# Performance work log

Measured on AMD Instinct MI355X. Metric: run time of the kernel, lower is better.

Reference implementation:

```python
import jax, jax.numpy as jnp
import numpy as np

V, D, H, L, MAXS = 32000, 768, 12, 6, 2048
HD = D // H  # 64
FF = 4 * D
B, S = 8, 1024
EPS = 1e-5


def _make_pe():
    pos = np.arange(MAXS, dtype=np.float32)[:, None]
    div = np.exp(np.arange(0, D, 2, dtype=np.float32) * (-np.log(10000.0) / D))
    pe = np.zeros((MAXS, D), dtype=np.float32)
    pe[:, 0::2] = np.sin(pos * div)
    pe[:, 1::2] = np.cos(pos * div)
    return jnp.asarray(pe)


def setup_inputs() -> dict:
    key = jax.random.key(0)
    ks = jax.random.split(key, 16)
    sc = 0.02
    return {
        "tokens": jax.random.randint(ks[0], (B, S), 0, V),
        "k_mask": jnp.ones((B, S), dtype=jnp.int32),
        "emb": jax.random.normal(ks[1], (V, D), jnp.float32) * sc,
        "pe": _make_pe(),
        "ln1_s": jnp.ones((L, D), jnp.float32),
        "ln1_b": jnp.zeros((L, D), jnp.float32),
        "wq": jax.random.normal(ks[2], (L, H, D, HD), jnp.float32) * sc,
        "wk": jax.random.normal(ks[3], (L, H, D, HD), jnp.float32) * sc,
        "wv": jax.random.normal(ks[4], (L, H, D, HD), jnp.float32) * sc,
        "wo": jax.random.normal(ks[5], (L, D, D), jnp.float32) * sc,
        "ln2_s": jnp.ones((L, D), jnp.float32),
        "ln2_b": jnp.zeros((L, D), jnp.float32),
        "w1": jax.random.normal(ks[6], (L, D, FF), jnp.float32) * sc,
        "b1": jnp.zeros((L, FF), jnp.float32),
        "w2": jax.random.normal(ks[7], (L, FF, D), jnp.float32) * sc,
        "b2": jnp.zeros((L, D), jnp.float32),
    }


def _ln(x, s, b):
    m = jnp.mean(x, axis=-1, keepdims=True)
    v = jnp.var(x, axis=-1, keepdims=True)
    return (x - m) * jax.lax.rsqrt(v + EPS) * s + b


def _forward(tokens, k_mask, emb, pe, ln1_s, ln1_b, wq, wk, wv, wo,
             ln2_s, ln2_b, w1, b1, w2, b2):
    x = emb[tokens] + pe[None, :tokens.shape[1], :]  # [B,S,D]
    mask = (k_mask != 0)[:, None, None, :]  # [B,1,1,S]
    for l in range(L):
        xn = _ln(x, ln1_s[l], ln1_b[l])
        q = jnp.einsum('bsd,hde->bhse', xn, wq[l])
        k = jnp.einsum('bsd,hde->bhse', xn, wk[l])
        v = jnp.einsum('bsd,hde->bhse', xn, wv[l])
        scores = jnp.einsum('bhse,bhte->bhst', q, k) / (HD ** 0.5)
        scores = jnp.where(mask, scores, -jnp.inf)
        attn = jax.nn.softmax(scores, axis=-1)
        o = jnp.einsum('bhst,bhte->bhse', attn, v)  # [B,H,S,HD]
        o = o.transpose(0, 2, 1, 3).reshape(x.shape)  # concat heads -> [B,S,D]
        x = x + o @ wo[l]
        xn = _ln(x, ln2_s[l], ln2_b[l])
        h = jax.nn.gelu(xn @ w1[l] + b1[l], approximate=False)
        x = x + h @ w2[l] + b2[l]
    return x


def reference(tokens, k_mask, emb, pe, ln1_s, ln1_b, wq, wk, wv, wo,
              ln2_s, ln2_b, w1, b1, w2, b2):
    return _forward(tokens, k_mask, emb, pe, ln1_s, ln1_b, wq, wk, wv, wo,
                    ln2_s, ln2_b, w1, b1, w2, b2)
```

## Files before the change

kernel.cpp:

```cpp
#include <hip/hip_runtime.h>
#include <math.h>

typedef unsigned short u16;
typedef unsigned int u32;
typedef __attribute__((ext_vector_type(8))) __bf16 bf16x8;
typedef __attribute__((ext_vector_type(4))) float f32x4;
typedef __attribute__((ext_vector_type(8))) unsigned short ushort8v;
typedef __attribute__((ext_vector_type(4))) float float4v;
typedef __attribute__((ext_vector_type(4))) unsigned short u16x4;

typedef const __attribute__((address_space(1))) void gvoid_t;
typedef __attribute__((address_space(3))) void lvoid_t;

#define MFMA(a, b, c) __builtin_amdgcn_mfma_f32_16x16x32_bf16((a), (b), (c), 0, 0, 0)

__device__ __forceinline__ u16 f2bf(float f) {
  __bf16 h = (__bf16)f;
  return __builtin_bit_cast(u16, h);
}

__device__ __forceinline__ void stage64(const u16* g, int ldg, u16* lds, int rows, int tid) {
  int w = tid >> 6, l = tid & 63;
  int lr = l >> 3;
  int cb = (l & 7) << 4;
  for (int it = 0; it < rows; it += 32) {
    int rbase = it + w * 8;
    int r = rbase + lr;
    int scb = cb ^ ((r & 7) << 4);
    const char* gp = (const char*)(g + (size_t)r * ldg) + scb;
    char* lp = (char*)lds + (size_t)rbase * 128;
    __builtin_amdgcn_global_load_lds((gvoid_t*)gp, (lvoid_t*)lp, 16, 0, 0);
  }
}

__device__ __forceinline__ bf16x8 ldsfrag(const u16* base, int row, int e0) {
  int boff = row * 128 + (((e0) << 1) ^ ((row & 7) << 4));
  return *(const bf16x8*)((const char*)base + boff);
}

__global__ void embed_kernel(const int* __restrict__ tok, const float* __restrict__ emb,
                             const float* __restrict__ pe, float* __restrict__ xf) {
  int row = blockIdx.x;
  int tid = threadIdx.x;
  int t = tok[row];
  int spos = row & 1023;
  float4v e = ((const float4v*)(emb + (size_t)t * 768))[tid];
  float4v p = ((const float4v*)(pe + (size_t)spos * 768))[tid];
  float4v r;
  r.x = e.x + p.x; r.y = e.y + p.y; r.z = e.z + p.z; r.w = e.w + p.w;
  ((float4v*)(xf + (size_t)row * 768))[tid] = r;
}

__global__ void ln_kernel(const float* __restrict__ x, const float* __restrict__ sc,
                          const float* __restrict__ bi, u16* __restrict__ out) {
  int row = blockIdx.x;
  int tid = threadIdx.x;
  float4v v = ((const float4v*)(x + (size_t)row * 768))[tid];
  float s = v.x + v.y + v.z + v.w;
  float s2 = v.x * v.x + v.y * v.y + v.z * v.z + v.w * v.w;
  #pragma unroll
  for (int off = 32; off >= 1; off >>= 1) {
    s += __shfl_down(s, off);
    s2 += __shfl_down(s2, off);
  }
  __shared__ float red[8];
  if ((tid & 63) == 0) { red[tid >> 6] = s; red[4 + (tid >> 6)] = s2; }
  __syncthreads();
  float S = red[0] + red[1] + red[2];
  float S2 = red[4] + red[5] + red[6];
  float m = S * (1.0f / 768.0f);
  float var = S2 * (1.0f / 768.0f) - m * m;
  float rs = rsqrtf(var + 1e-5f);
  float4v sv = ((const float4v*)sc)[tid];
  float4v bv = ((const float4v*)bi)[tid];
  u16x4 ov;
  ov.x = f2bf((v.x - m) * rs * sv.x + bv.x);
  ov.y = f2bf((v.y - m) * rs * sv.y + bv.y);
  ov.z = f2bf((v.z - m) * rs * sv.z + bv.z);
  ov.w = f2bf((v.w - m) * rs * sv.w + bv.w);
  *(u16x4*)(out + (size_t)row * 768 + tid * 4) = ov;
}

__global__ void convT_kernel(const float* __restrict__ src, u16* __restrict__ dst,
                             int N, int K, long long sz, long long dz) {
  src += (size_t)blockIdx.z * sz;
  dst += (size_t)blockIdx.z * dz;
  __shared__ float t[32][33];
  int n0 = blockIdx.x * 32, k0 = blockIdx.y * 32;
  int tid = threadIdx.x;
  int tx = tid & 31, ty = tid >> 5;
  for (int r = ty; r < 32; r += 8) t[r][tx] = src[(size_t)(k0 + r) * N + n0 + tx];
  __syncthreads();
  for (int r = ty; r < 32; r += 8) dst[(size_t)(n0 + r) * K + k0 + tx] = f2bf(t[tx][r]);
}

__global__ void convqkvT_kernel(const float* __restrict__ wq, const float* __restrict__ wk,
                                const float* __restrict__ wv, u16* __restrict__ dst,
                                long long wz, long long dz) {
  __shared__ float t[32][33];
  int n0 = blockIdx.x * 32, k0 = blockIdx.y * 32;
  int which = n0 / 768;
  int r0 = n0 % 768;
  int h = r0 >> 6, e0 = r0 & 63;
  const float* src = which == 0 ? wq : (which == 1 ? wk : wv);
  src += (size_t)blockIdx.z * wz;
  dst += (size_t)blockIdx.z * dz;
  int tid = threadIdx.x;
  int tx = tid & 31, ty = tid >> 5;
  for (int r = ty; r < 32; r += 8) t[r][tx] = src[(size_t)(h * 768 + k0 + r) * 64 + e0 + tx];
  __syncthreads();
  for (int r = ty; r < 32; r += 8) dst[(size_t)(n0 + r) * 768 + k0 + tx] = f2bf(t[tx][r]);
}

__global__ void transpose_v_kernel(const u16* __restrict__ v, u16* __restrict__ vt) {
  __shared__ u16 t[64][72];
  int bh = blockIdx.x, sc = blockIdx.y;
  int tid = threadIdx.x;
  const u16* src = v + ((size_t)bh * 1024 + sc * 64) * 64;
  int sl = tid >> 2, e0 = (tid & 3) * 16;
  ushort8v a = *(const ushort8v*)(src + (size_t)sl * 64 + e0);
  ushort8v b = *(const ushort8v*)(src + (size_t)sl * 64 + e0 + 8);
  #pragma unroll
  for (int j = 0; j < 8; ++j) t[sl][e0 + j] = a[j];
  #pragma unroll
  for (int j = 0; j < 8; ++j) t[sl][e0 + 8 + j] = b[j];
  __syncthreads();
  int e = tid >> 2, s0 = (tid & 3) * 16;
  ushort8v o0, o1;
  #pragma unroll
  for (int j = 0; j < 8; ++j) o0[j] = t[s0 + j][e];
  #pragma unroll
  for (int j = 0; j < 8; ++j) o1[j] = t[s0 + 8 + j][e];
  u16* dst = vt + ((size_t)bh * 64 + e) * 1024 + sc * 64 + s0;
  *(ushort8v*)dst = o0;
  *(ushort8v*)(dst + 8) = o1;
}

template <int MODE>
__global__ __launch_bounds__(256) void gemm128(
    const u16* __restrict__ A, int lda, const u16* __restrict__ Wt, int K,
    float* __restrict__ xf, u16* __restrict__ outb, const float* __restrict__ bias,
    u16* __restrict__ qb, u16* __restrict__ kb, u16* __restrict__ vb) {
  __shared__ alignas(16) u16 As[128 * 64];
  __shared__ alignas(16) u16 Bs[128 * 64];
  int tid = threadIdx.x, lane = tid & 63, w = tid >> 6;
  int wm = w >> 1, wn = w & 1;
  int m0 = blockIdx.x * 128, n0 = blockIdx.y * 128;
  f32x4 acc[4][4] = {};
  const u16* Ag = A + (size_t)m0 * lda;
  const u16* Bg = Wt + (size_t)n0 * K;
  int arow = wm * 64 + (lane & 15);
  int brow = wn * 64 + (lane & 15);
  int e0 = (lane >> 4) * 8;
  for (int kt = 0; kt < K; kt += 64) {
    __syncthreads();
    stage64(Ag + kt, lda, As, 128, tid);
    stage64(Bg + kt, K, Bs, 128, tid);
    __syncthreads();
    #pragma unroll
    for (int kk = 0; kk < 2; ++kk) {
      bf16x8 af[4], bfr[4];
      #pragma unroll
      for (int mt = 0; mt < 4; ++mt) af[mt] = ldsfrag(As, arow + mt * 16, kk * 32 + e0);
      #pragma unroll
      for (int nt = 0; nt < 4; ++nt) bfr[nt] = ldsfrag(Bs, brow + nt * 16, kk * 32 + e0);
      #pragma unroll
      for (int mt = 0; mt < 4; ++mt)
        #pragma unroll
        for (int nt = 0; nt < 4; ++nt)
          acc[mt][nt] = MFMA(af[mt], bfr[nt], acc[mt][nt]);
    }
  }
  int rbase = m0 + wm * 64 + ((lane >> 4) << 2);
  int cbase = n0 + wn * 64 + (lane & 15);
  if constexpr (MODE == 0) {
    int which = n0 / 768;
    u16* dstb = which == 0 ? qb : (which == 1 ? kb : vb);
    int cloc = cbase - which * 768;
    #pragma unroll
    for (int mt = 0; mt < 4; ++mt) {
      #pragma unroll
      for (int nt = 0; nt < 4; ++nt) {
        int rr = cloc + nt * 16;
        int h = rr >> 6, e = rr & 63;
        #pragma unroll
        for (int reg = 0; reg < 4; ++reg) {
          int row = rbase + mt * 16 + reg;
          int b = row >> 10, s = row & 1023;
          dstb[((size_t)(b * 12 + h) * 1024 + s) * 64 + e] = f2bf(acc[mt][nt][reg]);
        }
      }
    }
  } else {
    #pragma unroll
    for (int mt = 0; mt < 4; ++mt) {
      #pragma unroll
      for (int nt = 0; nt < 4; ++nt) {
        int col = cbase + nt * 16;
        #pragma unroll
        for (int reg = 0; reg < 4; ++reg) {
          int row = rbase + mt * 16 + reg;
          float val = acc[mt][nt][reg];
          if constexpr (MODE == 1) {
            xf[(size_t)row * 768 + col] += val;
          } else if constexpr (MODE == 2) {
            float t = val + bias[col];
            float u = t * fmaf(t * t, 0.044715f, 1.0f);
            float ex = __builtin_amdgcn_exp2f(u * -2.3022156f);
            float g = t * __builtin_amdgcn_rcpf(1.0f + ex);
            outb[(size_t)row * 3072 + col] = f2bf(g);
          } else {
            xf[(size_t)row * 768 + col] += val + bias[col];
          }
        }
      }
    }
  }
}

__global__ __launch_bounds__(256) void flash64(
    const u16* __restrict__ q, const u16* __restrict__ k, const u16* __restrict__ vt,
    const int* __restrict__ kmask, u16* __restrict__ o) {
  __shared__ alignas(16) u16 Qs[64 * 64];
  __shared__ alignas(16) u16 Ks[64 * 64];
  __shared__ alignas(16) u16 Vs[64 * 64];
  __shared__ alignas(16) u16 Ps[64 * 64];
  int tid = threadIdx.x, lane = tid & 63, w = tid >> 6;
  int lc = lane & 15;
  int bh = blockIdx.x, q0 = blockIdx.y * 64;
  int b = bh / 12, h = bh % 12;

  stage64(q + ((size_t)bh * 1024 + q0) * 64, 64, Qs, 64, tid);
  __syncthreads();
  int qrow = w * 16 + lc;
  int e0 = (lane >> 4) * 8;
  bf16x8 aq0 = ldsfrag(Qs, qrow, e0);
  bf16x8 aq1 = ldsfrag(Qs, qrow, 32 + e0);

  bf16x8 ones;
  #pragma unroll
  for (int j = 0; j < 8; ++j) ones[j] = (__bf16)1.0f;

  f32x4 oacc[4] = {};
  f32x4 lacc = {};
  const float SCL = 0.125f * 1.44269504f;
  const float SH = -3.0f * 1.44269504f;
  int prow_base = w * 16 + ((lane >> 4) << 2);

  for (int kt = 0; kt < 16; ++kt) {
    __syncthreads();
    stage64(k + ((size_t)bh * 1024 + kt * 64) * 64, 64, Ks, 64, tid);
    stage64(vt + (size_t)bh * 64 * 1024 + kt * 64, 1024, Vs, 64, tid);
    __syncthreads();

    f32x4 sacc[4] = {};
    #pragma unroll
    for (int nt = 0; nt < 4; ++nt) {
      bf16x8 bk = ldsfrag(Ks, nt * 16 + lc, e0);
      sacc[nt] = MFMA(aq0, bk, sacc[nt]);
    }
    #pragma unroll
    for (int nt = 0; nt < 4; ++nt) {
      bf16x8 bk = ldsfrag(Ks, nt * 16 + lc, 32 + e0);
      sacc[nt] = MFMA(aq1, bk, sacc[nt]);
    }

    #pragma unroll
    for (int nt = 0; nt < 4; ++nt) {
      int c = nt * 16 + lc;
      float mk = kmask[b * 1024 + kt * 64 + c] ? SH : -1e30f;
      #pragma unroll
      for (int r = 0; r < 4; ++r) {
        float p = __builtin_amdgcn_exp2f(fmaf(sacc[nt][r], SCL, mk));
        int prow = prow_base + r;
        int boff = prow * 128 + ((c << 1) ^ ((prow & 7) << 4));
        *(u16*)((char*)Ps + boff) = f2bf(p);
      }
    }

    bf16x8 ap0 = ldsfrag(Ps, qrow, e0);
    bf16x8 ap1 = ldsfrag(Ps, qrow, 32 + e0);
    lacc = MFMA(ap0, ones, lacc);
    lacc = MFMA(ap1, ones, lacc);
    #pragma unroll
    for (int et = 0; et < 4; ++et) {
      bf16x8 bv = ldsfrag(Vs, et * 16 + lc, e0);
      oacc[et] = MFMA(ap0, bv, oacc[et]);
    }
    #pragma unroll
    for (int et = 0; et < 4; ++et) {
      bf16x8 bv = ldsfrag(Vs, et * 16 + lc, 32 + e0);
      oacc[et] = MFMA(ap1, bv, oacc[et]);
    }
  }

  float rl[4];
  #pragma unroll
  for (int r = 0; r < 4; ++r) rl[r] = __builtin_amdgcn_rcpf(lacc[r]);
  int orow_base = q0 + prow_base;
  #pragma unroll
  for (int et = 0; et < 4; ++et) {
    int e = et * 16 + lc;
    #pragma unroll
    for (int r = 0; r < 4; ++r) {
      int row = orow_base + r;
      o[((size_t)(b * 1024 + row)) * 768 + h * 64 + e] = f2bf(oacc[et][r] * rl[r]);
    }
  }
}

__global__ void copy_kernel(const float* __restrict__ src, float* __restrict__ dst) {
  size_t i = (size_t)blockIdx.x * blockDim.x + threadIdx.x;
  ((float4v*)dst)[i] = ((const float4v*)src)[i];
}

extern "C" void kernel_launch(void* const* d_in, const int* in_sizes, int n_in,
                              void* d_out, int out_size, void* d_ws, size_t ws_size,
                              hipStream_t stream) {
  const int* tokens = (const int*)d_in[0];
  const int* kmask = (const int*)d_in[1];
  const float* emb = (const float*)d_in[2];
  const float* pe = (const float*)d_in[3];
  const float* ln1_s = (const float*)d_in[4];
  const float* ln1_b = (const float*)d_in[5];
  const float* wq = (const float*)d_in[6];
  const float* wk = (const float*)d_in[7];
  const float* wv = (const float*)d_in[8];
  const float* wo = (const float*)d_in[9];
  const float* ln2_s = (const float*)d_in[10];
  const float* ln2_b = (const float*)d_in[11];
  const float* w1 = (const float*)d_in[12];
  const float* b1 = (const float*)d_in[13];
  const float* w2 = (const float*)d_in[14];
  const float* b2 = (const float*)d_in[15];

  char* ws = (char*)d_ws;
  float* xf = (float*)ws;
  u16* xn   = (u16*)(ws + 25165824);
  u16* qb   = (u16*)(ws + 37748736);
  u16* kb   = (u16*)(ws + 50331648);
  u16* vb   = (u16*)(ws + 62914560);
  u16* vtb  = (u16*)(ws + 75497472);
  u16* ob   = (u16*)(ws + 88080384);
  u16* ffh  = (u16*)(ws + 100663296);

  const size_t SZ_QKV = (size_t)2304 * 768;
  const size_t SZ_O   = (size_t)768 * 768;
  const size_t SZ_F1  = (size_t)3072 * 768;
  const size_t SZ_F2  = (size_t)768 * 3072;
  const size_t NEED = 150994944 + 2 * 6 * (SZ_QKV + SZ_O + SZ_F1 + SZ_F2);
  bool pre = ws_size >= NEED;
  int nz = pre ? 6 : 1;
  u16* wqkvt = (u16*)(ws + 150994944);
  u16* wot   = wqkvt + (size_t)nz * SZ_QKV;
  u16* w1t   = wot + (size_t)nz * SZ_O;
  u16* w2t   = w1t + (size_t)nz * SZ_F1;

  embed_kernel<<<8192, 192, 0, stream>>>(tokens, emb, pe, xf);

  if (pre) {
    convqkvT_kernel<<<dim3(72, 24, 6), 256, 0, stream>>>(wq, wk, wv, wqkvt, 589824LL, (long long)SZ_QKV);
    convT_kernel<<<dim3(24, 24, 6), 256, 0, stream>>>(wo, wot, 768, 768, 589824LL, (long long)SZ_O);
    convT_kernel<<<dim3(96, 24, 6), 256, 0, stream>>>(w1, w1t, 3072, 768, 2359296LL, (long long)SZ_F1);
    convT_kernel<<<dim3(24, 96, 6), 256, 0, stream>>>(w2, w2t, 768, 3072, 2359296LL, (long long)SZ_F2);
  }

  for (int l = 0; l < 6; ++l) {
    size_t woff_qkv = (size_t)l * 12 * 768 * 64;
    size_t woff_o = (size_t)l * 768 * 768;
    size_t woff_ff = (size_t)l * 768 * 3072;
    const u16* wt_qkv_l = wqkvt + (pre ? (size_t)l * SZ_QKV : 0);
    const u16* wt_o_l   = wot   + (pre ? (size_t)l * SZ_O   : 0);
    const u16* wt_1_l   = w1t   + (pre ? (size_t)l * SZ_F1  : 0);
    const u16* wt_2_l   = w2t   + (pre ? (size_t)l * SZ_F2  : 0);

    if (!pre) {
      convqkvT_kernel<<<dim3(72, 24, 1), 256, 0, stream>>>(wq + woff_qkv, wk + woff_qkv, wv + woff_qkv, (u16*)wt_qkv_l, 0LL, 0LL);
      convT_kernel<<<dim3(24, 24, 1), 256, 0, stream>>>(wo + woff_o, (u16*)wt_o_l, 768, 768, 0LL, 0LL);
      convT_kernel<<<dim3(96, 24, 1), 256, 0, stream>>>(w1 + woff_ff, (u16*)wt_1_l, 3072, 768, 0LL, 0LL);
      convT_kernel<<<dim3(24, 96, 1), 256, 0, stream>>>(w2 + woff_ff, (u16*)wt_2_l, 768, 3072, 0LL, 0LL);
    }

    ln_kernel<<<8192, 192, 0, stream>>>(xf, ln1_s + l * 768, ln1_b + l * 768, xn);
    gemm128<0><<<dim3(64, 18), 256, 0, stream>>>(xn, 768, wt_qkv_l, 768, nullptr, nullptr, nullptr, qb, kb, vb);
    transpose_v_kernel<<<dim3(96, 16), 256, 0, stream>>>(vb, vtb);
    flash64<<<dim3(96, 16), 256, 0, stream>>>(qb, kb, vtb, kmask, ob);
    gemm128<1><<<dim3(64, 6), 256, 0, stream>>>(ob, 768, wt_o_l, 768, xf, nullptr, nullptr, nullptr, nullptr, nullptr);
    ln_kernel<<<8192, 192, 0, stream>>>(xf, ln2_s + l * 768, ln2_b + l * 768, xn);
    gemm128<2><<<dim3(64, 24), 256, 0, stream>>>(xn, 768, wt_1_l, 768, nullptr, ffh, b1 + l * 3072, nullptr, nullptr, nullptr);
    gemm128<3><<<dim3(64, 6), 256, 0, stream>>>(ffh, 3072, wt_2_l, 3072, xf, nullptr, b2 + l * 768, nullptr, nullptr, nullptr);
  }

  copy_kernel<<<6144, 256, 0, stream>>>(xf, (float*)d_out);
}
```

Baseline: 1.686 ms.

## Replace 128x128 GEMM with 256x256 multi-stage pipelined GEMM and split-K atomics

Replaces the 128x128 tile GEMM with a 256x256 tile, 512-thread kernel. It uses a 4-slot LDS ring with 3-stage-ahead global_load_lds prefetch, explicit vmcnt waits, and raised priority around the MFMA section. The residual-add GEMMs (attention output and FFN down projection) use split-K across three z-slices and accumulate into the fp32 residual with atomicAdd. The aim is more data reuse per tile, global loads overlapped with compute, and better occupancy for the small-N GEMMs. In exchange it adds atomic traffic, makes summation order nondeterministic, and drops the LDS swizzle, which may cause bank conflicts.

```diff
diff --git a/kernel.cpp b/kernel.cpp
--- a/kernel.cpp
+++ b/kernel.cpp
@@ -36,6 +36,17 @@
 __device__ __forceinline__ bf16x8 ldsfrag(const u16* base, int row, int e0) {
   int boff = row * 128 + (((e0) << 1) ^ ((row & 7) << 4));
   return *(const bf16x8*)((const char*)base + boff);
+}
+
+__device__ __forceinline__ void stage_slice512(const u16* g, int ldg, char* dst, int tid) {
+  int rr = tid >> 2, s = tid & 3;
+  char* lp = dst + (tid >> 6) * 1024;
+  #pragma unroll
+  for (int i = 0; i < 2; ++i) {
+    int row = i * 128 + rr;
+    const char* gp = (const char*)g + (size_t)row * (ldg * 2) + s * 16;
+    __builtin_amdgcn_global_load_lds((gvoid_t*)gp, (lvoid_t*)(lp + i * 8192), 16, 0, 0);
+  }
 }
 
 __global__ void embed_kernel(const int* __restrict__ tok, const float* __restrict__ emb,
@@ -137,51 +148,76 @@
 }
 
 template <int MODE>
-__global__ __launch_bounds__(256) void gemm128(
-    const u16* __restrict__ A, int lda, const u16* __restrict__ Wt, int K,
+__global__ __launch_bounds__(512, 1) void gemm256(
+    const u16* __restrict__ A, int lda, const u16* __restrict__ Wt, int ldb, int kChunk,
     float* __restrict__ xf, u16* __restrict__ outb, const float* __restrict__ bias,
     u16* __restrict__ qb, u16* __restrict__ kb, u16* __restrict__ vb) {
-  __shared__ alignas(16) u16 As[128 * 64];
-  __shared__ alignas(16) u16 Bs[128 * 64];
+  extern __shared__ char lds[];
   int tid = threadIdx.x, lane = tid & 63, w = tid >> 6;
-  int wm = w >> 1, wn = w & 1;
-  int m0 = blockIdx.x * 128, n0 = blockIdx.y * 128;
-  f32x4 acc[4][4] = {};
-  const u16* Ag = A + (size_t)m0 * lda;
-  const u16* Bg = Wt + (size_t)n0 * K;
-  int arow = wm * 64 + (lane & 15);
-  int brow = wn * 64 + (lane & 15);
-  int e0 = (lane >> 4) * 8;
-  for (int kt = 0; kt < K; kt += 64) {
-    __syncthreads();
-    stage64(Ag + kt, lda, As, 128, tid);
-    stage64(Bg + kt, K, Bs, 128, tid);
-    __syncthreads();
-    #pragma unroll
-    for (int kk = 0; kk < 2; ++kk) {
-      bf16x8 af[4], bfr[4];
+  int wm = w >> 2, wn = w & 3;
+  int m0 = blockIdx.x * 256, n0 = blockIdx.y * 256;
+  int kb0 = blockIdx.z * kChunk;
+  int NK = kChunk >> 5;
+  const u16* Ag = A + (size_t)m0 * lda + kb0;
+  const u16* Bg = Wt + (size_t)n0 * ldb + kb0;
+  f32x4 acc[8][4] = {};
+  int lcb = (lane >> 4) << 4;
+  int lc = lane & 15;
+
+  #pragma unroll
+  for (int p = 0; p < 3; ++p) {
+    stage_slice512(Ag + p * 32, lda, lds + (p & 3) * 32768, tid);
+    stage_slice512(Bg + p * 32, ldb, lds + (p & 3) * 32768 + 16384, tid);
+  }
+
+  for (int ks = 0; ks < NK; ++ks) {
+    int newer = NK - 1 - ks;
+    if (newer >= 2)      asm volatile("s_waitcnt vmcnt(8)" ::: "memory");
+    else if (newer == 1) asm volatile("s_waitcnt vmcnt(4)" ::: "memory");
+    else                 asm volatile("s_waitcnt vmcnt(0)" ::: "memory");
+    __builtin_amdgcn_sched_barrier(0);
+    __builtin_amdgcn_s_barrier();
+    __builtin_amdgcn_sched_barrier(0);
+
+    char* sa = lds + (ks & 3) * 32768;
+    char* sb = sa + 16384;
+    bf16x8 af[8], bfr[4];
+    #pragma unroll
+    for (int mt = 0; mt < 8; ++mt) {
+      int r = wm * 128 + mt * 16 + lc;
+      af[mt] = *(const bf16x8*)(sa + r * 64 + lcb);
+    }
+    #pragma unroll
+    for (int nt = 0; nt < 4; ++nt) {
+      int r = wn * 64 + nt * 16 + lc;
+      bfr[nt] = *(const bf16x8*)(sb + r * 64 + lcb);
+    }
+    if (ks + 3 < NK) {
+      stage_slice512(Ag + (ks + 3) * 32, lda, lds + ((ks + 3) & 3) * 32768, tid);
+      stage_slice512(Bg + (ks + 3) * 32, ldb, lds + ((ks + 3) & 3) * 32768 + 16384, tid);
+    }
+    asm volatile("s_waitcnt lgkmcnt(0)" ::: "memory");
+    __builtin_amdgcn_sched_barrier(0);
+    __builtin_amdgcn_s_setprio(1);
+    #pragma unroll
+    for (int mt = 0; mt < 8; ++mt)
       #pragma unroll
-      for (int mt = 0; mt < 4; ++mt) af[mt] = ldsfrag(As, arow + mt * 16, kk * 32 + e0);
-      #pragma unroll
-      for (int nt = 0; nt < 4; ++nt) bfr[nt] = ldsfrag(Bs, brow + nt * 16, kk * 32 + e0);
-      #pragma unroll
-      for (int mt = 0; mt < 4; ++mt)
-        #pragma unroll
-        for (int nt = 0; nt < 4; ++nt)
-          acc[mt][nt] = MFMA(af[mt], bfr[nt], acc[mt][nt]);
-    }
-  }
-  int rbase = m0 + wm * 64 + ((lane >> 4) << 2);
-  int cbase = n0 + wn * 64 + (lane & 15);
+      for (int nt = 0; nt < 4; ++nt)
+        acc[mt][nt] = MFMA(af[mt], bfr[nt], acc[mt][nt]);
+    __builtin_amdgcn_s_setprio(0);
+  }
+
+  int rbase = m0 + wm * 128 + ((lane >> 4) << 2);
+  int cbase = n0 + wn * 64 + lc;
   if constexpr (MODE == 0) {
     int which = n0 / 768;
     u16* dstb = which == 0 ? qb : (which == 1 ? kb : vb);
-    int cloc = cbase - which * 768;
-    #pragma unroll
-    for (int mt = 0; mt < 4; ++mt) {
+    int clocal = n0 - which * 768 + wn * 64 + lc;
+    #pragma unroll
+    for (int mt = 0; mt < 8; ++mt) {
       #pragma unroll
       for (int nt = 0; nt < 4; ++nt) {
-        int rr = cloc + nt * 16;
+        int rr = clocal + nt * 16;
         int h = rr >> 6, e = rr & 63;
         #pragma unroll
         for (int reg = 0; reg < 4; ++reg) {
@@ -191,27 +227,36 @@
         }
       }
     }
-  } else {
-    #pragma unroll
-    for (int mt = 0; mt < 4; ++mt) {
+  } else if constexpr (MODE == 2) {
+    #pragma unroll
+    for (int mt = 0; mt < 8; ++mt) {
       #pragma unroll
       for (int nt = 0; nt < 4; ++nt) {
         int col = cbase + nt * 16;
+        float bb = bias[col];
         #pragma unroll
         for (int reg = 0; reg < 4; ++reg) {
           int row = rbase + mt * 16 + reg;
-          float val = acc[mt][nt][reg];
-          if constexpr (MODE == 1) {
-            xf[(size_t)row * 768 + col] += val;
-          } else if constexpr (MODE == 2) {
-            float t = val + bias[col];
-            float u = t * fmaf(t * t, 0.044715f, 1.0f);
-            float ex = __builtin_amdgcn_exp2f(u * -2.3022156f);
-            float g = t * __builtin_amdgcn_rcpf(1.0f + ex);
-            outb[(size_t)row * 3072 + col] = f2bf(g);
-          } else {
-            xf[(size_t)row * 768 + col] += val + bias[col];
-          }
+          float t = acc[mt][nt][reg] + bb;
+          float u = t * fmaf(t * t, 0.044715f, 1.0f);
+          float ex = __builtin_amdgcn_exp2f(u * -2.3022156f);
+          float g = t * __builtin_amdgcn_rcpf(1.0f + ex);
+          outb[(size_t)row * 3072 + col] = f2bf(g);
+        }
+      }
+    }
+  } else {
+    bool addb = (MODE == 3) && (blockIdx.z == 0);
+    #pragma unroll
+    for (int mt = 0; mt < 8; ++mt) {
+      #pragma unroll
+      for (int nt = 0; nt < 4; ++nt) {
+        int col = cbase + nt * 16;
+        float bb = addb ? bias[col] : 0.0f;
+        #pragma unroll
+        for (int reg = 0; reg < 4; ++reg) {
+          int row = rbase + mt * 16 + reg;
+          atomicAdd(&xf[(size_t)row * 768 + col], acc[mt][nt][reg] + bb);
         }
       }
     }
@@ -334,6 +379,11 @@
   const float* w2 = (const float*)d_in[14];
   const float* b2 = (const float*)d_in[15];
 
+  (void)hipFuncSetAttribute((const void*)gemm256<0>, hipFuncAttributeMaxDynamicSharedMemorySize, 131072);
+  (void)hipFuncSetAttribute((const void*)gemm256<1>, hipFuncAttributeMaxDynamicSharedMemorySize, 131072);
+  (void)hipFuncSetAttribute((const void*)gemm256<2>, hipFuncAttributeMaxDynamicSharedMemorySize, 131072);
+  (void)hipFuncSetAttribute((const void*)gemm256<3>, hipFuncAttributeMaxDynamicSharedMemorySize, 131072);
+
   char* ws = (char*)d_ws;
   float* xf = (float*)ws;
   u16* xn   = (u16*)(ws + 25165824);
@@ -382,13 +432,13 @@
     }
 
     ln_kernel<<<8192, 192, 0, stream>>>(xf, ln1_s + l * 768, ln1_b + l * 768, xn);
-    gemm128<0><<<dim3(64, 18), 256, 0, stream>>>(xn, 768, wt_qkv_l, 768, nullptr, nullptr, nullptr, qb, kb, vb);
+    gemm256<0><<<dim3(32, 9, 1), 512, 131072, stream>>>(xn, 768, wt_qkv_l, 768, 768, nullptr, nullptr, nullptr, qb, kb, vb);
     transpose_v_kernel<<<dim3(96, 16), 256, 0, stream>>>(vb, vtb);
     flash64<<<dim3(96, 16), 256, 0, stream>>>(qb, kb, vtb, kmask, ob);
-    gemm128<1><<<dim3(64, 6), 256, 0, stream>>>(ob, 768, wt_o_l, 768, xf, nullptr, nullptr, nullptr, nullptr, nullptr);
+    gemm256<1><<<dim3(32, 3, 3), 512, 131072, stream>>>(ob, 768, wt_o_l, 768, 256, xf, nullptr, nullptr, nullptr, nullptr, nullptr);
     ln_kernel<<<8192, 192, 0, stream>>>(xf, ln2_s + l * 768, ln2_b + l * 768, xn);
-    gemm128<2><<<dim3(64, 24), 256, 0, stream>>>(xn, 768, wt_1_l, 768, nullptr, ffh, b1 + l * 3072, nullptr, nullptr, nullptr);
-    gemm128<3><<<dim3(64, 6), 256, 0, stream>>>(ffh, 3072, wt_2_l, 3072, xf, nullptr, b2 + l * 768, nullptr, nullptr, nullptr);
+    gemm256<2><<<dim3(32, 12, 1), 512, 131072, stream>>>(xn, 768, wt_1_l, 768, 768, nullptr, ffh, b1 + l * 3072, nullptr, nullptr, nullptr);
+    gemm256<3><<<dim3(32, 3, 3), 512, 131072, stream>>>(ffh, 3072, wt_2_l, 3072, 1024, xf, nullptr, b2 + l * 768, nullptr, nullptr, nullptr);
   }
 
   copy_kernel<<<6144, 256, 0, stream>>>(xf, (float*)d_out);
```

After: 2.288 ms. 35.7% more time.
